# Kernel optimization log

Measured on AMD Instinct MI355X. Metric: run time of the kernel, lower is better.

The kernel has to match this reference:

```python
import jax, jax.numpy as jnp
import numpy as np

N_LAYER = 6
N_EMBD = 768
N_HEAD = 12
BLOCK_SIZE = 256
SEG = 10
B = 2
T_SEG = 256  # t (== block_size here)


def setup_inputs() -> dict:
    key = jax.random.key(0)
    ks = iter(jax.random.split(key, 64))
    C, L = N_EMBD, N_LAYER
    d = {}
    for name in ['idx_up', 'idx_down', 'idx_lhand', 'idx_rhand', 'idx_transl',
                 'cond_music', 'cond_up', 'cond_down', 'cond_lhand', 'cond_rhand']:
        d[name] = jax.random.normal(next(ks), (B, T_SEG, C), dtype=jnp.float32)
    d['pos_emb'] = 0.02 * jax.random.normal(next(ks), (1, BLOCK_SIZE * SEG, C), dtype=jnp.float32)
    d['ln1_w'] = jnp.ones((L, C), jnp.float32)
    d['ln1_b'] = jnp.zeros((L, C), jnp.float32)
    d['ln2_w'] = jnp.ones((L, C), jnp.float32)
    d['ln2_b'] = jnp.zeros((L, C), jnp.float32)
    for nm in ['Wq', 'Wk', 'Wv', 'Wp']:
        d[nm] = 0.02 * jax.random.normal(next(ks), (L, C, C), dtype=jnp.float32)
    for nm in ['bq', 'bk', 'bv', 'bp']:
        d[nm] = jnp.zeros((L, C), jnp.float32)
    d['W1'] = 0.02 * jax.random.normal(next(ks), (L, 4 * C, C), dtype=jnp.float32)
    d['b1'] = jnp.zeros((L, 4 * C), jnp.float32)
    d['W2'] = 0.02 * jax.random.normal(next(ks), (L, C, 4 * C), dtype=jnp.float32)
    d['b2'] = jnp.zeros((L, C), jnp.float32)
    return d


def _layer_norm(x, w, b, eps=1e-5):
    mu = jnp.mean(x, axis=-1, keepdims=True)
    var = jnp.mean((x - mu) ** 2, axis=-1, keepdims=True)
    return (x - mu) * jax.lax.rsqrt(var + eps) * w + b


def _block(x, mask, ln1_w, ln1_b, Wq, bq, Wk, bk, Wv, bv, Wp, bp, ln2_w, ln2_b, W1, b1, W2, b2):
    Bq, T, C = x.shape
    H, hd = N_HEAD, C // N_HEAD
    h = _layer_norm(x, ln1_w, ln1_b)
    q = (h @ Wq.T + bq).reshape(Bq, T, H, hd).transpose(0, 2, 1, 3)  # [B,H,T,hd]
    k = (h @ Wk.T + bk).reshape(Bq, T, H, hd).transpose(0, 2, 1, 3)
    v = (h @ Wv.T + bv).reshape(Bq, T, H, hd).transpose(0, 2, 1, 3)
    att = jnp.einsum('bhqd,bhkd->bhqk', q, k) * (1.0 / np.sqrt(hd))
    att = jnp.where(mask == 0, -jnp.inf, att)
    att = jax.nn.softmax(att, axis=-1)
    y = jnp.einsum('bhqk,bhkd->bhqd', att, v).transpose(0, 2, 1, 3).reshape(Bq, T, C)
    x = x + (y @ Wp.T + bp)
    h2 = _layer_norm(x, ln2_w, ln2_b)
    h2 = jax.nn.gelu(h2 @ W1.T + b1, approximate=False) @ W2.T + b2
    return x + h2


def reference(idx_up, idx_down, idx_lhand, idx_rhand, idx_transl,
              cond_music, cond_up, cond_down, cond_lhand, cond_rhand,
              pos_emb, ln1_w, ln1_b, ln2_w, ln2_b,
              Wq, Wk, Wv, Wp, bq, bk, bv, bp, W1, b1, W2, b2):
    t = idx_up.shape[1]
    Tb = BLOCK_SIZE
    tok = jnp.concatenate([cond_music, cond_up, cond_down, cond_lhand, cond_rhand,
                           idx_up, idx_down, idx_lhand, idx_rhand, idx_transl], axis=1)
    pos = jnp.concatenate([pos_emb[:, s * Tb:s * Tb + t, :] for s in range(SEG)], axis=1)
    x = tok + pos
    # tiled block-causal mask: tril(t,t) repeated 10x10
    tri = jnp.tril(jnp.ones((t, t), jnp.float32))
    mask = jnp.tile(tri, (SEG, SEG))  # [T, T]
    for li in range(N_LAYER):
        x = _block(x, mask,
                   ln1_w[li], ln1_b[li], Wq[li], bq[li], Wk[li], bk[li],
                   Wv[li], bv[li], Wp[li], bp[li], ln2_w[li], ln2_b[li],
                   W1[li], b1[li], W2[li], b2[li])
    return x
```

## Files before the change

### kernel.cpp

```cpp
#include <hip/hip_runtime.h>
#include <hip/hip_bf16.h>
#include <stdint.h>
#include <stddef.h>

typedef unsigned short u16;
typedef __attribute__((ext_vector_type(8))) short bf16x8;
typedef __attribute__((ext_vector_type(4))) float f32x4;
typedef __attribute__((ext_vector_type(4))) unsigned short u16x4;

#define TC 768
#define TT 2560
#define NB 2
#define NM (NB * TT)
#define NH 12
#define HD 64
#define NL 6
#define LDQ 1536

static __device__ __forceinline__ u16 f2bf(float f) {
  return __builtin_bit_cast(u16, __float2bfloat16(f));
}

static __device__ __forceinline__ void gload16(const void* g, void* l) {
  __builtin_amdgcn_global_load_lds((const __attribute__((address_space(1))) void*)g,
                                   (__attribute__((address_space(3))) void*)l, 16, 0, 0);
}

__global__ __launch_bounds__(256) void embed_kernel(
    const float* __restrict__ cm, const float* __restrict__ cu, const float* __restrict__ cd,
    const float* __restrict__ cl, const float* __restrict__ cr,
    const float* __restrict__ iu, const float* __restrict__ id_, const float* __restrict__ il,
    const float* __restrict__ ir, const float* __restrict__ it,
    const float* __restrict__ pos, float* __restrict__ x)
{
  int v = blockIdx.x * 256 + threadIdx.x;
  const int NV = NM * TC / 4;
  if (v >= NV) return;
  int e = v * 4;
  int b = e / (TT * TC);
  int rem = e - b * (TT * TC);
  int tpos = rem / TC;
  int c = rem - tpos * TC;
  int s = tpos >> 8;
  int tt = tpos & 255;
  const float* src;
  switch (s) {
    case 0: src = cm; break; case 1: src = cu; break; case 2: src = cd; break;
    case 3: src = cl; break; case 4: src = cr; break; case 5: src = iu; break;
    case 6: src = id_; break; case 7: src = il; break; case 8: src = ir; break;
    default: src = it; break;
  }
  f32x4 a = *(const f32x4*)&src[(size_t)(b * 256 + tt) * TC + c];
  f32x4 p = *(const f32x4*)&pos[(size_t)tpos * TC + c];
  *(f32x4*)&x[e] = a + p;
}

__global__ __launch_bounds__(256) void conv_all_kernel(
    const float* __restrict__ Wq, const float* __restrict__ Wk, const float* __restrict__ Wv,
    const float* __restrict__ Wp, const float* __restrict__ W1, const float* __restrict__ W2,
    u16* __restrict__ wqkv, u16* __restrict__ wp, u16* __restrict__ w1, u16* __restrict__ w2)
{
  const int SQ = 768 * 768;
  int v = blockIdx.x * 256 + threadIdx.x;
  int e = v * 4;
  const float* src; u16* dst;
  if (e < 3 * SQ) {
    int wsel = e / SQ; int le = e - wsel * SQ;
    src = (wsel == 0 ? Wq : wsel == 1 ? Wk : Wv) + le;
    dst = wqkv + e;
  } else if (e < 4 * SQ) {
    src = Wp + (e - 3 * SQ); dst = wp + (e - 3 * SQ);
  } else if (e < 8 * SQ) {
    src = W1 + (e - 4 * SQ); dst = w1 + (e - 4 * SQ);
  } else {
    src = W2 + (e - 8 * SQ); dst = w2 + (e - 8 * SQ);
  }
  f32x4 f = *(const f32x4*)src;
  u16x4 r;
  r[0] = f2bf(f[0]); r[1] = f2bf(f[1]); r[2] = f2bf(f[2]); r[3] = f2bf(f[3]);
  *(u16x4*)dst = r;
}

__global__ __launch_bounds__(256) void ln_kernel(
    const float* __restrict__ x, const float* __restrict__ w, const float* __restrict__ bb,
    u16* __restrict__ out)
{
  int row = blockIdx.x;
  int tid = threadIdx.x;
  const float* xr = x + (size_t)row * TC;
  float v0 = xr[tid], v1 = xr[tid + 256], v2 = xr[tid + 512];
  float s = v0 + v1 + v2;
  float ss = v0 * v0 + v1 * v1 + v2 * v2;
  #pragma unroll
  for (int m = 1; m < 64; m <<= 1) { s += __shfl_xor(s, m, 64); ss += __shfl_xor(ss, m, 64); }
  __shared__ float red[8];
  int wave = tid >> 6, lane = tid & 63;
  if (lane == 0) { red[wave] = s; red[4 + wave] = ss; }
  __syncthreads();
  s = red[0] + red[1] + red[2] + red[3];
  ss = red[4] + red[5] + red[6] + red[7];
  const float inv = 1.0f / 768.0f;
  float mu = s * inv;
  float var = ss * inv - mu * mu;
  float rs = rsqrtf(var + 1e-5f);
  size_t o = (size_t)row * TC + tid;
  out[o]       = f2bf((v0 - mu) * rs * w[tid]       + bb[tid]);
  out[o + 256] = f2bf((v1 - mu) * rs * w[tid + 256] + bb[tid + 256]);
  out[o + 512] = f2bf((v2 - mu) * rs * w[tid + 512] + bb[tid + 512]);
}

template<int EPI, int TM>
__global__ __launch_bounds__(256) void gemm_kernel(
    const u16* __restrict__ A, const u16* __restrict__ Bw,
    const float* __restrict__ b0, const float* __restrict__ b1, const float* __restrict__ b2,
    u16* __restrict__ outb, float* __restrict__ resid, u16* __restrict__ vTout, int K, int N)
{
  constexpr int NR = (TM == 128) ? 4 : 2;
  constexpr int NLD = (TM == 128) ? 8 : 6;
  __shared__ __align__(16) u16 As[2][TM * 64];
  __shared__ __align__(16) u16 Bs[2][128 * 64];
  const int bm = blockIdx.x, bn = blockIdx.y;
  const int tid = threadIdx.x;
  const int wave = tid >> 6;
  const int lane = tid & 63;
  const int wr = (TM == 128) ? (wave >> 1) : 0;
  const int wc = (TM == 128) ? (wave & 1) : wave;
  const int WCS = (TM == 128) ? 64 : 32;
  const int l15 = lane & 15, l16 = lane >> 4;

  f32x4 acc[4][NR];
  #pragma unroll
  for (int m = 0; m < 4; ++m)
    #pragma unroll
    for (int n = 0; n < NR; ++n) acc[m][n] = f32x4{0.f, 0.f, 0.f, 0.f};

  const u16* gA0 = A + (size_t)(bm * TM) * K;
  const u16* gB0 = Bw + (size_t)(bn * 128) * K;

  #define GSTAGE(BUF, KT)                                                       \
    {                                                                           \
      const u16* ga = gA0 + (size_t)(KT) * 64;                                  \
      const u16* gb = gB0 + (size_t)(KT) * 64;                                  \
      _Pragma("unroll")                                                         \
      for (int i = 0; i < TM / 32; ++i) {                                       \
        int s = i * 256 + tid; int row = s >> 3; int c = (s & 7) ^ (row & 7);   \
        gload16(ga + (size_t)row * K + c * 8, &As[BUF][s * 8]);                 \
      }                                                                         \
      _Pragma("unroll")                                                         \
      for (int i = 0; i < 4; ++i) {                                             \
        int s = i * 256 + tid; int row = s >> 3; int c = (s & 7) ^ (row & 7);   \
        gload16(gb + (size_t)row * K + c * 8, &Bs[BUF][s * 8]);                 \
      }                                                                         \
    }

  const int nkt = K >> 6;
  GSTAGE(0, 0)

  for (int kt = 0; kt < nkt; ++kt) {
    const int cb = kt & 1;
    if (kt + 1 < nkt) {
      GSTAGE(cb ^ 1, kt + 1)
      asm volatile("s_waitcnt vmcnt(%0)" :: "i"(NLD) : "memory");
    } else {
      asm volatile("s_waitcnt vmcnt(0)" ::: "memory");
    }
    __builtin_amdgcn_s_barrier();
    __builtin_amdgcn_sched_barrier(0);
    #pragma unroll
    for (int kk = 0; kk < 2; ++kk) {
      bf16x8 aF[4], bF[NR];
      #pragma unroll
      for (int m = 0; m < 4; ++m) {
        int row = wr * 64 + m * 16 + l15;
        aF[m] = *(const bf16x8*)&As[cb][row * 64 + (((kk * 4 + l16) ^ (row & 7)) * 8)];
      }
      #pragma unroll
      for (int n = 0; n < NR; ++n) {
        int row = wc * WCS + n * 16 + l15;
        bF[n] = *(const bf16x8*)&Bs[cb][row * 64 + (((kk * 4 + l16) ^ (row & 7)) * 8)];
      }
      __builtin_amdgcn_s_setprio(1);
      #pragma unroll
      for (int m = 0; m < 4; ++m)
        #pragma unroll
        for (int n = 0; n < NR; ++n)
          acc[m][n] = __builtin_amdgcn_mfma_f32_16x16x32_bf16(aF[m], bF[n], acc[m][n], 0, 0, 0);
      __builtin_amdgcn_s_setprio(0);
    }
    __builtin_amdgcn_sched_barrier(0);
    __builtin_amdgcn_s_barrier();
  }
  #undef GSTAGE

  #pragma unroll
  for (int m = 0; m < 4; ++m) {
    int row = bm * TM + wr * 64 + m * 16 + l16 * 4;
    #pragma unroll
    for (int n = 0; n < NR; ++n) {
      int col = bn * 128 + wc * WCS + n * 16 + l15;
      float bv;
      if (EPI == 0) bv = (col < 768) ? b0[col] : (col < 1536 ? b1[col - 768] : b2[col - 1536]);
      else          bv = b0[col];
      if (EPI == 0) {
        if (col < 1536) {
          float sc = (col < 768) ? 0.180336880f : 1.0f;
          #pragma unroll
          for (int r = 0; r < 4; ++r)
            outb[(size_t)(row + r) * LDQ + col] = f2bf((acc[m][n][r] + bv) * sc);
        } else {
          int cc = col - 1536, hh = cc >> 6, dd = cc & 63;
          int bb2 = row / TT, t = row - bb2 * TT;
          int k6 = t & 63;
          int c6 = k6 >> 4, g6 = (k6 >> 2) & 3;
          int tp = (t & ~63) | ((c6 & 2) << 4) | (g6 << 3) | ((c6 & 1) << 2);
          u16x4 pk;
          #pragma unroll
          for (int r = 0; r < 4; ++r) pk[r] = f2bf(acc[m][n][r] + bv);
          *(u16x4*)&vTout[((size_t)(bb2 * NH + hh) * HD + dd) * TT + tp] = pk;
        }
      } else {
        #pragma unroll
        for (int r = 0; r < 4; ++r) {
          float v = acc[m][n][r] + bv;
          if (EPI == 1) {
            float g = 0.5f * v * (1.0f + erff(v * 0.70710678118654752f));
            outb[(size_t)(row + r) * N + col] = f2bf(g);
          } else {
            resid[(size_t)(row + r) * N + col] += v;
          }
        }
      }
    }
  }
}

__global__ __launch_bounds__(256, 8) void attn_kernel(
    const u16* __restrict__ qk, const u16* __restrict__ vT, u16* __restrict__ yb)
{
  __shared__ __align__(16) u16 Ks[2][64 * 64];
  __shared__ __align__(16) u16 Vs[2][64 * 64];
  const int tid = threadIdx.x;
  const int wave = tid >> 6, lane = tid & 63;
  const int l15 = lane & 15, l16 = lane >> 4;
  const int idx = blockIdx.x;
  const int g = idx / 24;
  const int bh = idx - g * 24;
  const int jd = 3 - (g / 10);
  const int qt = (g - (3 - jd) * 10) * 4 + jd;
  const int b = bh / NH, h = bh - (bh / NH) * NH;
  const int q0 = qt * 64 + wave * 16;
  const int qloc = wave * 16 + l15;

  const u16* qb = qk + (size_t)b * TT * LDQ + h * HD;
  const u16* kb = qb + 768;
  const u16* vt = vT + (size_t)(b * NH + h) * HD * TT;

  bf16x8 qB0 = *(const bf16x8*)&qb[(size_t)(q0 + l15) * LDQ + l16 * 8];
  bf16x8 qB1 = *(const bf16x8*)&qb[(size_t)(q0 + l15) * LDQ + 32 + l16 * 8];

  f32x4 o[4];
  #pragma unroll
  for (int n = 0; n < 4; ++n) o[n] = f32x4{0.f, 0.f, 0.f, 0.f};
  float lrun = 0.f;

  const int sl0 = tid >> 3;
  const int sp  = tid & 7;

  #define STAGE(BUF, K0)                                                            \
    {                                                                               \
      _Pragma("unroll")                                                             \
      for (int rr = 0; rr < 2; ++rr) {                                              \
        int row = rr * 32 + sl0;                                                    \
        int sl = sp ^ (row & 7);                                                    \
        int slot = row * 8 + sp;                                                    \
        gload16(&kb[(size_t)((K0) + row) * LDQ + sl * 8], &Ks[BUF][slot * 8]);      \
        gload16(&vt[(size_t)row * TT + (K0) + sl * 8], &Vs[BUF][slot * 8]);         \
      }                                                                             \
    }

  STAGE(0, 0)
  int cur = 0;

  union U { u16x4 h[2]; bf16x8 v; };

  for (int ks = 0; ks < 10; ++ks) {
    for (int j = 0; j <= jd; ++j) {
      const bool last = (ks == 9) && (j == jd);
      if (!last) {
        int nk0 = (j < jd) ? ks * 256 + (j + 1) * 64 : (ks + 1) * 256;
        STAGE(cur ^ 1, nk0)
        asm volatile("s_waitcnt vmcnt(4)" ::: "memory");
      } else {
        asm volatile("s_waitcnt vmcnt(0)" ::: "memory");
      }
      __builtin_amdgcn_s_barrier();
      __builtin_amdgcn_sched_barrier(0);

      f32x4 s[4];
      __builtin_amdgcn_s_setprio(1);
      #pragma unroll
      for (int c = 0; c < 4; ++c) {
        int row = c * 16 + l15, sw = row & 7;
        bf16x8 k0f = *(const bf16x8*)&Ks[cur][row * 64 + ((l16 ^ sw) * 8)];
        bf16x8 k1f = *(const bf16x8*)&Ks[cur][row * 64 + (((4 + l16) ^ sw) * 8)];
        f32x4 z = __builtin_amdgcn_mfma_f32_16x16x32_bf16(k0f, qB0, f32x4{0.f,0.f,0.f,0.f}, 0, 0, 0);
        s[c] = __builtin_amdgcn_mfma_f32_16x16x32_bf16(k1f, qB1, z, 0, 0, 0);
      }
      __builtin_amdgcn_s_setprio(0);

      if (j == jd) {
        #pragma unroll
        for (int c = 0; c < 4; ++c)
          #pragma unroll
          for (int r = 0; r < 4; ++r)
            if (c * 16 + l16 * 4 + r > qloc) s[c][r] = -1e30f;
      }

      float ts = 0.f;
      #pragma unroll
      for (int c = 0; c < 4; ++c)
        #pragma unroll
        for (int r = 0; r < 4; ++r) {
          float p = exp2f(s[c][r] - 8.0f);
          s[c][r] = p;
          ts += p;
        }
      ts += __shfl_xor(ts, 16, 64);
      ts += __shfl_xor(ts, 32, 64);
      lrun += ts;

      u16x4 wcp[4];
      #pragma unroll
      for (int c = 0; c < 4; ++c) {
        wcp[c][0] = f2bf(s[c][0]); wcp[c][1] = f2bf(s[c][1]);
        wcp[c][2] = f2bf(s[c][2]); wcp[c][3] = f2bf(s[c][3]);
      }
      U p0, p1;
      p0.h[0] = wcp[0]; p0.h[1] = wcp[1];
      p1.h[0] = wcp[2]; p1.h[1] = wcp[3];
      __builtin_amdgcn_s_setprio(1);
      #pragma unroll
      for (int mt = 0; mt < 4; ++mt) {
        int row = mt * 16 + l15, sw = row & 7;
        const u16* vrow = &Vs[cur][row * 64];
        bf16x8 v0 = *(const bf16x8*)&vrow[(l16 ^ sw) * 8];
        bf16x8 v1 = *(const bf16x8*)&vrow[((4 + l16) ^ sw) * 8];
        o[mt] = __builtin_amdgcn_mfma_f32_16x16x32_bf16(v0, p0.v, o[mt], 0, 0, 0);
        o[mt] = __builtin_amdgcn_mfma_f32_16x16x32_bf16(v1, p1.v, o[mt], 0, 0, 0);
      }
      __builtin_amdgcn_s_setprio(0);
      __builtin_amdgcn_sched_barrier(0);
      __builtin_amdgcn_s_barrier();
      cur ^= 1;
    }
  }
  #undef STAGE

  float invl = 1.0f / lrun;
  u16* yr = &yb[(size_t)(b * TT + q0 + l15) * TC + h * HD];
  #pragma unroll
  for (int mt = 0; mt < 4; ++mt) {
    u16x4 pk;
    pk[0] = f2bf(o[mt][0] * invl); pk[1] = f2bf(o[mt][1] * invl);
    pk[2] = f2bf(o[mt][2] * invl); pk[3] = f2bf(o[mt][3] * invl);
    *(u16x4*)&yr[mt * 16 + l16 * 4] = pk;
  }
}

extern "C" void kernel_launch(void* const* d_in, const int* in_sizes, int n_in,
                              void* d_out, int out_size, void* d_ws, size_t ws_size,
                              hipStream_t stream)
{
  (void)in_sizes; (void)n_in; (void)out_size; (void)ws_size;
  const float* IU = (const float*)d_in[0];
  const float* ID = (const float*)d_in[1];
  const float* IL = (const float*)d_in[2];
  const float* IR = (const float*)d_in[3];
  const float* IT = (const float*)d_in[4];
  const float* CM = (const float*)d_in[5];
  const float* CU = (const float*)d_in[6];
  const float* CD = (const float*)d_in[7];
  const float* CL = (const float*)d_in[8];
  const float* CR = (const float*)d_in[9];
  const float* POS = (const float*)d_in[10];
  const float* LN1W = (const float*)d_in[11];
  const float* LN1B = (const float*)d_in[12];
  const float* LN2W = (const float*)d_in[13];
  const float* LN2B = (const float*)d_in[14];
  const float* WQ = (const float*)d_in[15];
  const float* WK = (const float*)d_in[16];
  const float* WV = (const float*)d_in[17];
  const float* WP = (const float*)d_in[18];
  const float* BQ = (const float*)d_in[19];
  const float* BK = (const float*)d_in[20];
  const float* BV = (const float*)d_in[21];
  const float* BP = (const float*)d_in[22];
  const float* W1 = (const float*)d_in[23];
  const float* B1 = (const float*)d_in[24];
  const float* W2 = (const float*)d_in[25];
  const float* B2 = (const float*)d_in[26];

  float* x = (float*)d_out;
  char* ws = (char*)d_ws;
  u16* ws_wqkv = (u16*)(ws + 0);
  u16* ws_wp   = (u16*)(ws + 3538944);
  u16* ws_w1   = (u16*)(ws + 4718592);
  u16* ws_w2   = (u16*)(ws + 9437184);
  u16* ws_h    = (u16*)(ws + 14155776);
  u16* ws_qkv  = (u16*)(ws + 22020096);
  u16* ws_vt   = (u16*)(ws + 37748736);
  u16* ws_y    = (u16*)(ws + 45613056);
  u16* ws_g    = ws_qkv;

  embed_kernel<<<(NM * TC / 4) / 256, 256, 0, stream>>>(CM, CU, CD, CL, CR, IU, ID, IL, IR, IT, POS, x);

  const int SQ = 768 * 768;
  const int W1SL = 3072 * 768;
  for (int li = 0; li < NL; ++li) {
    conv_all_kernel<<<6912, 256, 0, stream>>>(
        WQ + (size_t)li * SQ, WK + (size_t)li * SQ, WV + (size_t)li * SQ,
        WP + (size_t)li * SQ, W1 + (size_t)li * W1SL, W2 + (size_t)li * W1SL,
        ws_wqkv, ws_wp, ws_w1, ws_w2);

    ln_kernel<<<NM, 256, 0, stream>>>(x, LN1W + li * TC, LN1B + li * TC, ws_h);
    gemm_kernel<0, 128><<<dim3(NM / 128, 2304 / 128), 256, 0, stream>>>(
        ws_h, ws_wqkv, BQ + li * TC, BK + li * TC, BV + li * TC, ws_qkv, nullptr, ws_vt, 768, 2304);
    attn_kernel<<<dim3(40 * 24), 256, 0, stream>>>(ws_qkv, ws_vt, ws_y);
    gemm_kernel<2, 64><<<dim3(NM / 64, 768 / 128), 256, 0, stream>>>(
        ws_y, ws_wp, BP + li * TC, nullptr, nullptr, nullptr, x, nullptr, 768, 768);
    ln_kernel<<<NM, 256, 0, stream>>>(x, LN2W + li * TC, LN2B + li * TC, ws_h);
    gemm_kernel<1, 128><<<dim3(NM / 128, 3072 / 128), 256, 0, stream>>>(
        ws_h, ws_w1, B1 + (size_t)li * 3072, nullptr, nullptr, ws_g, nullptr, nullptr, 768, 3072);
    gemm_kernel<2, 64><<<dim3(NM / 64, 768 / 128), 256, 0, stream>>>(
        ws_g, ws_w2, B2 + li * TC, nullptr, nullptr, nullptr, x, nullptr, 3072, 768);
  }
}
```

Measured before the change: 1.312 ms.

## Use 256x256 GEMM tiles for QKV and FC1, vectorize layernorm

The QKV and FC1 GEMMs move from 128x128 tiles with 256 threads to 256x256 tiles with 512 threads and 8x4 MFMA accumulators per wave. This roughly doubles arithmetic intensity per LDS byte and cuts global reloads of A and B. The residual-add GEMMs are split into a dedicated 64x128 kernel. Layernorm now uses 192 threads with float4 loads and packed bf16 stores. Bigger tiles need 128KB of LDS and many registers, so occupancy drops. The grids also get small: the QKV GEMM launches 20x9=180 blocks, which may underfill the CUs.

```diff
diff --git a/kernel.cpp b/kernel.cpp
--- a/kernel.cpp
+++ b/kernel.cpp
@@ -81,86 +81,83 @@
   *(u16x4*)dst = r;
 }
 
-__global__ __launch_bounds__(256) void ln_kernel(
+__global__ __launch_bounds__(192) void ln_kernel(
     const float* __restrict__ x, const float* __restrict__ w, const float* __restrict__ bb,
     u16* __restrict__ out)
 {
   int row = blockIdx.x;
   int tid = threadIdx.x;
-  const float* xr = x + (size_t)row * TC;
-  float v0 = xr[tid], v1 = xr[tid + 256], v2 = xr[tid + 512];
-  float s = v0 + v1 + v2;
-  float ss = v0 * v0 + v1 * v1 + v2 * v2;
+  f32x4 v = *(const f32x4*)&x[(size_t)row * TC + tid * 4];
+  float s = v[0] + v[1] + v[2] + v[3];
+  float ss = v[0] * v[0] + v[1] * v[1] + v[2] * v[2] + v[3] * v[3];
   #pragma unroll
   for (int m = 1; m < 64; m <<= 1) { s += __shfl_xor(s, m, 64); ss += __shfl_xor(ss, m, 64); }
-  __shared__ float red[8];
+  __shared__ float red[6];
   int wave = tid >> 6, lane = tid & 63;
-  if (lane == 0) { red[wave] = s; red[4 + wave] = ss; }
+  if (lane == 0) { red[wave] = s; red[3 + wave] = ss; }
   __syncthreads();
-  s = red[0] + red[1] + red[2] + red[3];
-  ss = red[4] + red[5] + red[6] + red[7];
+  s = red[0] + red[1] + red[2];
+  ss = red[3] + red[4] + red[5];
   const float inv = 1.0f / 768.0f;
   float mu = s * inv;
   float var = ss * inv - mu * mu;
   float rs = rsqrtf(var + 1e-5f);
-  size_t o = (size_t)row * TC + tid;
-  out[o]       = f2bf((v0 - mu) * rs * w[tid]       + bb[tid]);
-  out[o + 256] = f2bf((v1 - mu) * rs * w[tid + 256] + bb[tid + 256]);
-  out[o + 512] = f2bf((v2 - mu) * rs * w[tid + 512] + bb[tid + 512]);
-}
-
-template<int EPI, int TM>
-__global__ __launch_bounds__(256) void gemm_kernel(
+  f32x4 wv = *(const f32x4*)&w[tid * 4];
+  f32x4 bv = *(const f32x4*)&bb[tid * 4];
+  u16x4 o4;
+  #pragma unroll
+  for (int j = 0; j < 4; ++j) o4[j] = f2bf((v[j] - mu) * rs * wv[j] + bv[j]);
+  *(u16x4*)&out[(size_t)row * TC + tid * 4] = o4;
+}
+
+template<int EPI>
+__global__ __launch_bounds__(512, 2) void gemm256_kernel(
     const u16* __restrict__ A, const u16* __restrict__ Bw,
     const float* __restrict__ b0, const float* __restrict__ b1, const float* __restrict__ b2,
-    u16* __restrict__ outb, float* __restrict__ resid, u16* __restrict__ vTout, int K, int N)
-{
-  constexpr int NR = (TM == 128) ? 4 : 2;
-  constexpr int NLD = (TM == 128) ? 8 : 6;
-  __shared__ __align__(16) u16 As[2][TM * 64];
-  __shared__ __align__(16) u16 Bs[2][128 * 64];
+    u16* __restrict__ outb, u16* __restrict__ vTout, int K, int N)
+{
+  __shared__ __align__(16) u16 As[2][256 * 64];
+  __shared__ __align__(16) u16 Bs[2][256 * 64];
   const int bm = blockIdx.x, bn = blockIdx.y;
   const int tid = threadIdx.x;
   const int wave = tid >> 6;
   const int lane = tid & 63;
-  const int wr = (TM == 128) ? (wave >> 1) : 0;
-  const int wc = (TM == 128) ? (wave & 1) : wave;
-  const int WCS = (TM == 128) ? 64 : 32;
+  const int wr = wave >> 2, wc = wave & 3;
   const int l15 = lane & 15, l16 = lane >> 4;
 
-  f32x4 acc[4][NR];
-  #pragma unroll
-  for (int m = 0; m < 4; ++m)
+  f32x4 acc[8][4];
+  #pragma unroll
+  for (int m = 0; m < 8; ++m)
     #pragma unroll
-    for (int n = 0; n < NR; ++n) acc[m][n] = f32x4{0.f, 0.f, 0.f, 0.f};
-
-  const u16* gA0 = A + (size_t)(bm * TM) * K;
-  const u16* gB0 = Bw + (size_t)(bn * 128) * K;
-
-  #define GSTAGE(BUF, KT)                                                       \
-    {                                                                           \
-      const u16* ga = gA0 + (size_t)(KT) * 64;                                  \
-      const u16* gb = gB0 + (size_t)(KT) * 64;                                  \
-      _Pragma("unroll")                                                         \
-      for (int i = 0; i < TM / 32; ++i) {                                       \
-        int s = i * 256 + tid; int row = s >> 3; int c = (s & 7) ^ (row & 7);   \
-        gload16(ga + (size_t)row * K + c * 8, &As[BUF][s * 8]);                 \
-      }                                                                         \
-      _Pragma("unroll")                                                         \
-      for (int i = 0; i < 4; ++i) {                                             \
-        int s = i * 256 + tid; int row = s >> 3; int c = (s & 7) ^ (row & 7);   \
-        gload16(gb + (size_t)row * K + c * 8, &Bs[BUF][s * 8]);                 \
-      }                                                                         \
+    for (int n = 0; n < 4; ++n) acc[m][n] = f32x4{0.f, 0.f, 0.f, 0.f};
+
+  const u16* gA0 = A + (size_t)(bm * 256) * K;
+  const u16* gB0 = Bw + (size_t)(bn * 256) * K;
+
+  #define GSTAGE256(BUF, KT)                                                     \
+    {                                                                            \
+      const u16* ga = gA0 + (size_t)(KT) * 64;                                   \
+      const u16* gb = gB0 + (size_t)(KT) * 64;                                   \
+      _Pragma("unroll")                                                          \
+      for (int i = 0; i < 4; ++i) {                                              \
+        int s = i * 512 + tid; int row = s >> 3; int c = (s & 7) ^ (row & 7);    \
+        gload16(ga + (size_t)row * K + c * 8, &As[BUF][s * 8]);                  \
+      }                                                                          \
+      _Pragma("unroll")                                                          \
+      for (int i = 0; i < 4; ++i) {                                              \
+        int s = i * 512 + tid; int row = s >> 3; int c = (s & 7) ^ (row & 7);    \
+        gload16(gb + (size_t)row * K + c * 8, &Bs[BUF][s * 8]);                  \
+      }                                                                          \
     }
 
   const int nkt = K >> 6;
-  GSTAGE(0, 0)
+  GSTAGE256(0, 0)
 
   for (int kt = 0; kt < nkt; ++kt) {
     const int cb = kt & 1;
     if (kt + 1 < nkt) {
-      GSTAGE(cb ^ 1, kt + 1)
-      asm volatile("s_waitcnt vmcnt(%0)" :: "i"(NLD) : "memory");
+      GSTAGE256(cb ^ 1, kt + 1)
+      asm volatile("s_waitcnt vmcnt(8)" ::: "memory");
     } else {
       asm volatile("s_waitcnt vmcnt(0)" ::: "memory");
     }
@@ -168,40 +165,38 @@
     __builtin_amdgcn_sched_barrier(0);
     #pragma unroll
     for (int kk = 0; kk < 2; ++kk) {
-      bf16x8 aF[4], bF[NR];
-      #pragma unroll
-      for (int m = 0; m < 4; ++m) {
-        int row = wr * 64 + m * 16 + l15;
+      bf16x8 aF[8], bF[4];
+      #pragma unroll
+      for (int m = 0; m < 8; ++m) {
+        int row = wr * 128 + m * 16 + l15;
         aF[m] = *(const bf16x8*)&As[cb][row * 64 + (((kk * 4 + l16) ^ (row & 7)) * 8)];
       }
       #pragma unroll
-      for (int n = 0; n < NR; ++n) {
-        int row = wc * WCS + n * 16 + l15;
+      for (int n = 0; n < 4; ++n) {
+        int row = wc * 64 + n * 16 + l15;
         bF[n] = *(const bf16x8*)&Bs[cb][row * 64 + (((kk * 4 + l16) ^ (row & 7)) * 8)];
       }
       __builtin_amdgcn_s_setprio(1);
       #pragma unroll
-      for (int m = 0; m < 4; ++m)
+      for (int m = 0; m < 8; ++m)
         #pragma unroll
-        for (int n = 0; n < NR; ++n)
+        for (int n = 0; n < 4; ++n)
           acc[m][n] = __builtin_amdgcn_mfma_f32_16x16x32_bf16(aF[m], bF[n], acc[m][n], 0, 0, 0);
       __builtin_amdgcn_s_setprio(0);
     }
     __builtin_amdgcn_sched_barrier(0);
     __builtin_amdgcn_s_barrier();
   }
-  #undef GSTAGE
-
-  #pragma unroll
-  for (int m = 0; m < 4; ++m) {
-    int row = bm * TM + wr * 64 + m * 16 + l16 * 4;
+  #undef GSTAGE256
+
+  #pragma unroll
+  for (int m = 0; m < 8; ++m) {
+    int row = bm * 256 + wr * 128 + m * 16 + l16 * 4;
     #pragma unroll
-    for (int n = 0; n < NR; ++n) {
-      int col = bn * 128 + wc * WCS + n * 16 + l15;
-      float bv;
-      if (EPI == 0) bv = (col < 768) ? b0[col] : (col < 1536 ? b1[col - 768] : b2[col - 1536]);
-      else          bv = b0[col];
+    for (int n = 0; n < 4; ++n) {
+      int col = bn * 256 + wc * 64 + n * 16 + l15;
       if (EPI == 0) {
+        float bv = (col < 768) ? b0[col] : (col < 1536 ? b1[col - 768] : b2[col - 1536]);
         if (col < 1536) {
           float sc = (col < 768) ? 0.180336880f : 1.0f;
           #pragma unroll
@@ -219,17 +214,105 @@
           *(u16x4*)&vTout[((size_t)(bb2 * NH + hh) * HD + dd) * TT + tp] = pk;
         }
       } else {
+        float bv = b0[col];
         #pragma unroll
         for (int r = 0; r < 4; ++r) {
           float v = acc[m][n][r] + bv;
-          if (EPI == 1) {
-            float g = 0.5f * v * (1.0f + erff(v * 0.70710678118654752f));
-            outb[(size_t)(row + r) * N + col] = f2bf(g);
-          } else {
-            resid[(size_t)(row + r) * N + col] += v;
-          }
+          float g = 0.5f * v * (1.0f + erff(v * 0.70710678118654752f));
+          outb[(size_t)(row + r) * N + col] = f2bf(g);
         }
       }
+    }
+  }
+}
+
+__global__ __launch_bounds__(256) void gemm64_kernel(
+    const u16* __restrict__ A, const u16* __restrict__ Bw,
+    const float* __restrict__ b0, float* __restrict__ resid, int K, int N)
+{
+  __shared__ __align__(16) u16 As[2][64 * 64];
+  __shared__ __align__(16) u16 Bs[2][128 * 64];
+  const int bm = blockIdx.x, bn = blockIdx.y;
+  const int tid = threadIdx.x;
+  const int wave = tid >> 6;
+  const int lane = tid & 63;
+  const int wc = wave;
+  const int l15 = lane & 15, l16 = lane >> 4;
+
+  f32x4 acc[4][2];
+  #pragma unroll
+  for (int m = 0; m < 4; ++m)
+    #pragma unroll
+    for (int n = 0; n < 2; ++n) acc[m][n] = f32x4{0.f, 0.f, 0.f, 0.f};
+
+  const u16* gA0 = A + (size_t)(bm * 64) * K;
+  const u16* gB0 = Bw + (size_t)(bn * 128) * K;
+
+  #define GSTAGE64(BUF, KT)                                                      \
+    {                                                                            \
+      const u16* ga = gA0 + (size_t)(KT) * 64;                                   \
+      const u16* gb = gB0 + (size_t)(KT) * 64;                                   \
+      _Pragma("unroll")                                                          \
+      for (int i = 0; i < 2; ++i) {                                              \
+        int s = i * 256 + tid; int row = s >> 3; int c = (s & 7) ^ (row & 7);    \
+        gload16(ga + (size_t)row * K + c * 8, &As[BUF][s * 8]);                  \
+      }                                                                          \
+      _Pragma("unroll")                                                          \
+      for (int i = 0; i < 4; ++i) {                                              \
+        int s = i * 256 + tid; int row = s >> 3; int c = (s & 7) ^ (row & 7);    \
+        gload16(gb + (size_t)row * K + c * 8, &Bs[BUF][s * 8]);                  \
+      }                                                                          \
+    }
+
+  const int nkt = K >> 6;
+  GSTAGE64(0, 0)
+
+  for (int kt = 0; kt < nkt; ++kt) {
+    const int cb = kt & 1;
+    if (kt + 1 < nkt) {
+      GSTAGE64(cb ^ 1, kt + 1)
+      asm volatile("s_waitcnt vmcnt(6)" ::: "memory");
+    } else {
+      asm volatile("s_waitcnt vmcnt(0)" ::: "memory");
+    }
+    __builtin_amdgcn_s_barrier();
+    __builtin_amdgcn_sched_barrier(0);
+    #pragma unroll
+    for (int kk = 0; kk < 2; ++kk) {
+      bf16x8 aF[4], bF[2];
+      #pragma unroll
+      for (int m = 0; m < 4; ++m) {
+        int row = m * 16 + l15;
+        aF[m] = *(const bf16x8*)&As[cb][row * 64 + (((kk * 4 + l16) ^ (row & 7)) * 8)];
+      }
+      #pragma unroll
+      for (int n = 0; n < 2; ++n) {
+        int row = wc * 32 + n * 16 + l15;
+        bF[n] = *(const bf16x8*)&Bs[cb][row * 64 + (((kk * 4 + l16) ^ (row & 7)) * 8)];
+      }
+      __builtin_amdgcn_s_setprio(1);
+      #pragma unroll
+      for (int m = 0; m < 4; ++m)
+        #pragma unroll
+        for (int n = 0; n < 2; ++n)
+          acc[m][n] = __builtin_amdgcn_mfma_f32_16x16x32_bf16(aF[m], bF[n], acc[m][n], 0, 0, 0);
+      __builtin_amdgcn_s_setprio(0);
+    }
+    __builtin_amdgcn_sched_barrier(0);
+    __builtin_amdgcn_s_barrier();
+  }
+  #undef GSTAGE64
+
+  #pragma unroll
+  for (int m = 0; m < 4; ++m) {
+    int row = bm * 64 + m * 16 + l16 * 4;
+    #pragma unroll
+    for (int n = 0; n < 2; ++n) {
+      int col = bn * 128 + wc * 32 + n * 16 + l15;
+      float bv = b0[col];
+      #pragma unroll
+      for (int r = 0; r < 4; ++r)
+        resid[(size_t)(row + r) * N + col] += acc[m][n][r] + bv;
     }
   }
 }
@@ -422,16 +505,16 @@
         WP + (size_t)li * SQ, W1 + (size_t)li * W1SL, W2 + (size_t)li * W1SL,
         ws_wqkv, ws_wp, ws_w1, ws_w2);
 
-    ln_kernel<<<NM, 256, 0, stream>>>(x, LN1W + li * TC, LN1B + li * TC, ws_h);
-    gemm_kernel<0, 128><<<dim3(NM / 128, 2304 / 128), 256, 0, stream>>>(
-        ws_h, ws_wqkv, BQ + li * TC, BK + li * TC, BV + li * TC, ws_qkv, nullptr, ws_vt, 768, 2304);
+    ln_kernel<<<NM, 192, 0, stream>>>(x, LN1W + li * TC, LN1B + li * TC, ws_h);
+    gemm256_kernel<0><<<dim3(NM / 256, 2304 / 256), 512, 0, stream>>>(
+        ws_h, ws_wqkv, BQ + li * TC, BK + li * TC, BV + li * TC, ws_qkv, ws_vt, 768, 2304);
     attn_kernel<<<dim3(40 * 24), 256, 0, stream>>>(ws_qkv, ws_vt, ws_y);
-    gemm_kernel<2, 64><<<dim3(NM / 64, 768 / 128), 256, 0, stream>>>(
-        ws_y, ws_wp, BP + li * TC, nullptr, nullptr, nullptr, x, nullptr, 768, 768);
-    ln_kernel<<<NM, 256, 0, stream>>>(x, LN2W + li * TC, LN2B + li * TC, ws_h);
-    gemm_kernel<1, 128><<<dim3(NM / 128, 3072 / 128), 256, 0, stream>>>(
-        ws_h, ws_w1, B1 + (size_t)li * 3072, nullptr, nullptr, ws_g, nullptr, nullptr, 768, 3072);
-    gemm_kernel<2, 64><<<dim3(NM / 64, 768 / 128), 256, 0, stream>>>(
-        ws_g, ws_w2, B2 + li * TC, nullptr, nullptr, nullptr, x, nullptr, 3072, 768);
-  }
-}
+    gemm64_kernel<<<dim3(NM / 64, 768 / 128), 256, 0, stream>>>(
+        ws_y, ws_wp, BP + li * TC, x, 768, 768);
+    ln_kernel<<<NM, 192, 0, stream>>>(x, LN2W + li * TC, LN2B + li * TC, ws_h);
+    gemm256_kernel<1><<<dim3(NM / 256, 3072 / 256), 512, 0, stream>>>(
+        ws_h, ws_w1, B1 + (size_t)li * 3072, nullptr, nullptr, ws_g, nullptr, 768, 3072);
+    gemm64_kernel<<<dim3(NM / 64, 768 / 128), 256, 0, stream>>>(
+        ws_g, ws_w2, B2 + li * TC, x, 3072, 768);
+  }
+}
```

Result: no change. 1.324 ms (+0.9%).
